# Performance work log

Hardware: AMD Instinct MI355X
Metric: run time of the kernel (lower is better)

## Reference

```python
import jax, jax.numpy as jnp
import numpy as np

N = 50000   # nodes
E = 600000  # directed edges
B = 128     # graphs
IN = 128
H = 128
K = 30      # sort-pool k
C_OUT = 32
KER = 5
OUT_DIM = 10
L_OUT = K - KER + 1  # 26


def setup_inputs() -> dict:
    key = jax.random.key(0)
    ks = jax.random.split(key, 12)
    s = 0.05
    return {
        "x": jax.random.normal(ks[0], (N, IN), jnp.float32),
        "edge_index": jax.random.randint(ks[1], (2, E), 0, N),
        "batch": jnp.sort(jax.random.randint(ks[2], (N,), 0, B)),
        "W0": jax.random.normal(ks[3], (IN, H), jnp.float32) * s,
        "b0": jnp.zeros((H,), jnp.float32),
        "W1": jax.random.normal(ks[4], (H, H), jnp.float32) * s,
        "b1": jnp.zeros((H,), jnp.float32),
        "W2": jax.random.normal(ks[5], (H, H), jnp.float32) * s,
        "b2": jnp.zeros((H,), jnp.float32),
        "conv_w": jax.random.normal(ks[6], (C_OUT, H, KER), jnp.float32) * s,
        "conv_b": jnp.zeros((C_OUT,), jnp.float32),
        "lin1_w": jax.random.normal(ks[7], (C_OUT * L_OUT, H), jnp.float32) * s,
        "lin1_b": jnp.zeros((H,), jnp.float32),
        "lin2_w": jax.random.normal(ks[8], (H, OUT_DIM), jnp.float32) * s,
        "lin2_b": jnp.zeros((OUT_DIM,), jnp.float32),
    }


def reference(x, edge_index, batch, W0, b0, W1, b1, W2, b2,
              conv_w, conv_b, lin1_w, lin1_b, lin2_w, lin2_b):
    # --- GCN normalization (A + I, symmetric deg^-1/2) ---
    loops = jnp.arange(N)
    row = jnp.concatenate([edge_index[0], loops])  # source
    col = jnp.concatenate([edge_index[1], loops])  # target (aggregation side)
    deg = jax.ops.segment_sum(jnp.ones_like(col, dtype=x.dtype), col, num_segments=N)
    dinv = jax.lax.rsqrt(jnp.maximum(deg, 1.0))
    norm = dinv[row] * dinv[col]  # [E+N]

    def gcn(h, W, b):
        hw = h @ W                                            # [N,H]
        msg = hw[row] * norm[:, None]                         # gather [E+N,H]
        return jax.ops.segment_sum(msg, col, num_segments=N) + b

    h = jax.nn.relu(gcn(x, W0, b0))
    h = jax.nn.relu(gcn(h, W1, b1))
    h = jax.nn.relu(gcn(h, W2, b2))

    # --- SortAggregation: per-graph sort by last channel (desc), top-K, zero-pad ---
    last = h[:, -1]
    order = jnp.lexsort((-last, batch))  # primary: batch, secondary: last desc
    hs = h[order]
    bs = batch[order]
    counts = jax.ops.segment_sum(jnp.ones((N,), jnp.int32), batch, num_segments=B)
    starts = jnp.cumsum(counts) - counts  # exclusive prefix sum
    rank = jnp.arange(N) - starts[bs]     # within-graph rank after sort
    r = jnp.where(rank < K, rank, K)      # overflow bucket K is discarded
    pooled = jnp.zeros((B, K + 1, H), h.dtype).at[bs, r].add(hs)[:, :K]  # [B,K,H]

    # --- conv1d head (NCH layout, matches torch view/transpose) ---
    xc = jnp.transpose(pooled, (0, 2, 1))  # [B,H,K]
    y = jax.lax.conv_general_dilated(xc, conv_w, (1,), "VALID",
                                     dimension_numbers=("NCH", "OIH", "NCH"))
    y = jax.nn.relu(y + conv_b[None, :, None])  # [B,C_OUT,L_OUT]
    y = y.reshape(B, -1)
    y = jax.nn.relu(y @ lin1_w + lin1_b)
    return y @ lin2_w + lin2_b  # [B,OUT_DIM]
```

## Files before the change

kernel.cpp:

```cpp
#include <hip/hip_runtime.h>
#include <math.h>

#define Nn 50000
#define Ee 600000
#define Bg 128
#define Hd 128
#define Kt 30
#define CO 32
#define KW 5
#define LOUT 26
#define CAP 2048
#define SCB 196
#define MMB 782

typedef float v2f __attribute__((ext_vector_type(2)));
typedef short bf16x8 __attribute__((ext_vector_type(8)));
typedef float f32x4 __attribute__((ext_vector_type(4)));

__device__ __forceinline__ unsigned short bfr(float v) {
    unsigned u = __builtin_bit_cast(unsigned, v);
    unsigned r = (u + 0x7FFFu + ((u >> 16) & 1u)) >> 16;
    return (unsigned short)r;
}
__device__ __forceinline__ float bff(unsigned short h) {
    unsigned u = ((unsigned)h) << 16;
    return __builtin_bit_cast(float, u);
}

__global__ void countpack_kernel(const int* __restrict__ ei, const int* __restrict__ batch,
                            int* __restrict__ deg_i, int* __restrict__ bstart,
                            const float* __restrict__ conv_w, float* __restrict__ wT2,
                            const float* __restrict__ W0, const float* __restrict__ W1,
                            const float* __restrict__ W2,
                            ushort* __restrict__ Bph, ushort* __restrict__ Bpm,
                            ushort* __restrict__ Bpl) {
    int i = blockIdx.x * 256 + threadIdx.x;
    if (i < Ee) atomicAdd(&deg_i[ei[Ee + i]], 1);
    if (i < Nn) {
        int b = batch[i];
        if (i == 0) bstart[b] = 0;
        else if (batch[i - 1] != b) bstart[b] = i;
    }
    if (i == 0) bstart[Bg] = Nn;
    if (i < CO * KW * Hd) {
        int ci = i & 127;
        int r = i >> 7;
        int o = r / KW, k = r - o * KW;
        wT2[i] = conv_w[((size_t)o * Hd + ci) * KW + k];
    }
    if (i < 3 * 2048) {
        int l = i >> 11;
        int r = i & 2047;
        int kc = r >> 9;
        int n = (r >> 6) & 7;
        int lane = r & 63;
        int m = lane & 15, kq = lane >> 4;
        const float* W = (l == 0) ? W0 : (l == 1) ? W1 : W2;
        int col = n * 16 + m;
        size_t off = ((size_t)l * 2048 + (size_t)((kc * 8 + n) * 64 + lane)) * 8;
#pragma unroll
        for (int j = 0; j < 8; ++j) {
            float v = W[(size_t)(kc * 32 + kq * 8 + j) * Hd + col];
            unsigned short h = bfr(v);
            float r1 = v - bff(h);
            unsigned short mid = bfr(r1);
            Bph[off + j] = h;
            Bpm[off + j] = mid;
            Bpl[off + j] = bfr(r1 - bff(mid));
        }
    }
}

__global__ __launch_bounds__(256) void scanBC2_kernel(const int* __restrict__ deg_i,
                            int* __restrict__ row_ptr, float* __restrict__ dinv,
                            int* __restrict__ bstart) {
    __shared__ int ls[256];
    __shared__ int boffS;
    int tid = threadIdx.x;
    int b = blockIdx.x;
    int s = 0;
    for (int k = 0; k < b; ++k)
        s += deg_i[k * 256 + tid] + 1;
    ls[tid] = s;
    __syncthreads();
    for (int off = 128; off > 0; off >>= 1) {
        if (tid < off) ls[tid] += ls[tid + off];
        __syncthreads();
    }
    if (tid == 0) boffS = ls[0];
    __syncthreads();
    int boff = boffS;
    int i = b * 256 + tid;
    int v2 = 0;
    if (i < Nn) {
        int raw = deg_i[i];
        v2 = raw + 1;
        dinv[i] = 1.0f / sqrtf((float)(raw + 2));
    }
    ls[tid] = v2;
    __syncthreads();
    for (int off = 1; off < 256; off <<= 1) {
        int t = (tid >= off) ? ls[tid - off] : 0;
        __syncthreads();
        ls[tid] += t;
        __syncthreads();
    }
    if (i < Nn) row_ptr[i + 1] = ls[tid] + boff;
    if (i == 0) row_ptr[0] = 0;
    if (b == 0 && tid == 0) {
        for (int bb = Bg - 1; bb >= 0; --bb)
            if (bstart[bb] == -1) bstart[bb] = bstart[bb + 1];
    }
}

__device__ __forceinline__ void mmx_body(int bid, int tid,
                            const float* __restrict__ Hin,
                            const ushort* __restrict__ Bph, const ushort* __restrict__ Bpm,
                            const ushort* __restrict__ Bpl,
                            const float* __restrict__ dinv, float* __restrict__ hw) {
    int w = tid >> 6, lane = tid & 63;
    int m = lane & 15, kq = lane >> 4;
    int rowA = bid * 64 + w * 16 + m;
    bool va = rowA < Nn;
    const float* ap = Hin + (size_t)rowA * Hd;
    f32x4 acc[8];
#pragma unroll
    for (int n = 0; n < 8; ++n) acc[n] = (f32x4)0.f;
#pragma unroll
    for (int kc = 0; kc < 4; ++kc) {
        bf16x8 a0 = (bf16x8)0, a1 = (bf16x8)0, a2 = (bf16x8)0;
        if (va) {
            float av[8];
            *(float4*)&av[0] = *(const float4*)(ap + kc * 32 + kq * 8);
            *(float4*)&av[4] = *(const float4*)(ap + kc * 32 + kq * 8 + 4);
#pragma unroll
            for (int j = 0; j < 8; ++j) {
                unsigned short h = bfr(av[j]);
                float r1 = av[j] - bff(h);
                unsigned short mid = bfr(r1);
                a0[j] = (short)h;
                a1[j] = (short)mid;
                a2[j] = (short)bfr(r1 - bff(mid));
            }
        }
        const ushort* bhp = Bph + (size_t)((kc * 8) * 64 + lane) * 8;
        const ushort* bmp = Bpm + (size_t)((kc * 8) * 64 + lane) * 8;
        const ushort* blp = Bpl + (size_t)((kc * 8) * 64 + lane) * 8;
#pragma unroll
        for (int n = 0; n < 8; ++n) {
            bf16x8 b0 = *(const bf16x8*)(bhp + (size_t)n * 64 * 8);
            bf16x8 b1 = *(const bf16x8*)(bmp + (size_t)n * 64 * 8);
            bf16x8 b2 = *(const bf16x8*)(blp + (size_t)n * 64 * 8);
            acc[n] = __builtin_amdgcn_mfma_f32_16x16x32_bf16(a0, b0, acc[n], 0, 0, 0);
            acc[n] = __builtin_amdgcn_mfma_f32_16x16x32_bf16(a1, b0, acc[n], 0, 0, 0);
            acc[n] = __builtin_amdgcn_mfma_f32_16x16x32_bf16(a0, b1, acc[n], 0, 0, 0);
            acc[n] = __builtin_amdgcn_mfma_f32_16x16x32_bf16(a1, b1, acc[n], 0, 0, 0);
            acc[n] = __builtin_amdgcn_mfma_f32_16x16x32_bf16(a2, b0, acc[n], 0, 0, 0);
            acc[n] = __builtin_amdgcn_mfma_f32_16x16x32_bf16(a0, b2, acc[n], 0, 0, 0);
        }
    }
    int rbase = bid * 64 + w * 16 + kq * 4;
#pragma unroll
    for (int reg = 0; reg < 4; ++reg) {
        int r = rbase + reg;
        if (r < Nn) {
            float s = dinv[r];
#pragma unroll
            for (int n = 0; n < 8; ++n)
                hw[(size_t)r * Hd + n * 16 + m] = acc[n][reg] * s;
        }
    }
}

__global__ __launch_bounds__(256) void mmxfill_kernel(const float* __restrict__ Hin,
                            const ushort* __restrict__ Bph, const ushort* __restrict__ Bpm,
                            const ushort* __restrict__ Bpl,
                            const float* __restrict__ dinv, float* __restrict__ hw,
                            const int* __restrict__ ei, const int* __restrict__ row_ptr,
                            int* __restrict__ cnt, int* __restrict__ csr_src) {
    if (blockIdx.x < MMB) {
        mmx_body(blockIdx.x, threadIdx.x, Hin, Bph, Bpm, Bpl, dinv, hw);
    } else {
        int e = (blockIdx.x - MMB) * 256 + threadIdx.x;
        if (e < Ee) {
            int c = ei[Ee + e];
            int r = ei[e];
            int p = row_ptr[c] + atomicAdd(&cnt[c], 1) + 1;
            csr_src[p] = r;
        }
    }
}

__global__ __launch_bounds__(256) void aggmm_kernel(const float* __restrict__ hwin,
                            const int* __restrict__ row_ptr, const int* __restrict__ csr_src,
                            const float* __restrict__ dinv, const float* __restrict__ bias,
                            const ushort* __restrict__ Bph, const ushort* __restrict__ Bpm,
                            const ushort* __restrict__ Bpl,
                            float* __restrict__ hwout) {
    __shared__ __align__(16) float At[64][132];
    int tid = threadIdx.x;
    int w = tid >> 6, lane = tid & 63;
    int bid = blockIdx.x;
    const v2f* hw2 = (const v2f*)hwin;
    v2f bv = ((const v2f*)bias)[lane];
    for (int t = 0; t < 16; ++t) {
        int rl = w * 16 + t;
        int node = bid * 64 + rl;
        v2f o = (v2f)0.f;
        if (node < Nn) {
            v2f a0 = hw2[(size_t)node * 64 + lane];
            v2f a1 = (v2f)0.f, a2 = (v2f)0.f, a3 = (v2f)0.f;
            int e0 = row_ptr[node], e1 = row_ptr[node + 1];
            int e = e0;
            for (; e + 3 < e1; e += 4) {
                int s0 = __builtin_nontemporal_load(csr_src + e);
                int s1 = __builtin_nontemporal_load(csr_src + e + 1);
                int s2 = __builtin_nontemporal_load(csr_src + e + 2);
                int s3 = __builtin_nontemporal_load(csr_src + e + 3);
                a0 += hw2[(size_t)s0 * 64 + lane];
                a1 += hw2[(size_t)s1 * 64 + lane];
                a2 += hw2[(size_t)s2 * 64 + lane];
                a3 += hw2[(size_t)s3 * 64 + lane];
            }
            for (; e < e1; ++e) {
                int s0 = __builtin_nontemporal_load(csr_src + e);
                a0 += hw2[(size_t)s0 * 64 + lane];
            }
            v2f acc = (a0 + a1) + (a2 + a3);
            float d = dinv[node];
            o.x = fmaxf(fmaf(d, acc.x, bv.x), 0.f);
            o.y = fmaxf(fmaf(d, acc.y, bv.y), 0.f);
        }
        *(v2f*)&At[rl][lane * 2] = o;
    }
    int m = lane & 15, kq = lane >> 4;
    f32x4 acc[8];
#pragma unroll
    for (int n = 0; n < 8; ++n) acc[n] = (f32x4)0.f;
    const float* arow = &At[w * 16 + m][0];
#pragma unroll
    for (int kc = 0; kc < 4; ++kc) {
        bf16x8 a0, a1, a2;
        float av[8];
        *(float4*)&av[0] = *(const float4*)(arow + kc * 32 + kq * 8);
        *(float4*)&av[4] = *(const float4*)(arow + kc * 32 + kq * 8 + 4);
#pragma unroll
        for (int j = 0; j < 8; ++j) {
            unsigned short h = bfr(av[j]);
            float r1 = av[j] - bff(h);
            unsigned short mid = bfr(r1);
            a0[j] = (short)h;
            a1[j] = (short)mid;
            a2[j] = (short)bfr(r1 - bff(mid));
        }
        const ushort* bhp = Bph + (size_t)((kc * 8) * 64 + lane) * 8;
        const ushort* bmp = Bpm + (size_t)((kc * 8) * 64 + lane) * 8;
        const ushort* blp = Bpl + (size_t)((kc * 8) * 64 + lane) * 8;
#pragma unroll
        for (int n = 0; n < 8; ++n) {
            bf16x8 b0 = *(const bf16x8*)(bhp + (size_t)n * 64 * 8);
            bf16x8 b1 = *(const bf16x8*)(bmp + (size_t)n * 64 * 8);
            bf16x8 b2 = *(const bf16x8*)(blp + (size_t)n * 64 * 8);
            acc[n] = __builtin_amdgcn_mfma_f32_16x16x32_bf16(a0, b0, acc[n], 0, 0, 0);
            acc[n] = __builtin_amdgcn_mfma_f32_16x16x32_bf16(a1, b0, acc[n], 0, 0, 0);
            acc[n] = __builtin_amdgcn_mfma_f32_16x16x32_bf16(a0, b1, acc[n], 0, 0, 0);
            acc[n] = __builtin_amdgcn_mfma_f32_16x16x32_bf16(a1, b1, acc[n], 0, 0, 0);
            acc[n] = __builtin_amdgcn_mfma_f32_16x16x32_bf16(a2, b0, acc[n], 0, 0, 0);
            acc[n] = __builtin_amdgcn_mfma_f32_16x16x32_bf16(a0, b2, acc[n], 0, 0, 0);
        }
    }
    int rbase = bid * 64 + w * 16 + kq * 4;
#pragma unroll
    for (int reg = 0; reg < 4; ++reg) {
        int r = rbase + reg;
        if (r < Nn) {
            float s = dinv[r];
#pragma unroll
            for (int n = 0; n < 8; ++n)
                hwout[(size_t)r * Hd + n * 16 + m] = acc[n][reg] * s;
        }
    }
}

__global__ __launch_bounds__(256) void agg_kernel(const float* __restrict__ hw,
                            const int* __restrict__ row_ptr, const int* __restrict__ csr_src,
                            const float* __restrict__ dinv, const float* __restrict__ bias,
                            float* __restrict__ hout) {
    int node = blockIdx.x * 4 + (threadIdx.x >> 6);
    if (node >= Nn) return;
    int lane = threadIdx.x & 63;
    const v2f* hw2 = (const v2f*)hw;
    v2f a0 = hw2[(size_t)node * 64 + lane];
    v2f a1 = 0.f, a2 = 0.f, a3 = 0.f;
    int e0 = row_ptr[node], e1 = row_ptr[node + 1];
    int e = e0;
    for (; e + 3 < e1; e += 4) {
        int s0 = __builtin_nontemporal_load(csr_src + e);
        int s1 = __builtin_nontemporal_load(csr_src + e + 1);
        int s2 = __builtin_nontemporal_load(csr_src + e + 2);
        int s3 = __builtin_nontemporal_load(csr_src + e + 3);
        a0 += hw2[(size_t)s0 * 64 + lane];
        a1 += hw2[(size_t)s1 * 64 + lane];
        a2 += hw2[(size_t)s2 * 64 + lane];
        a3 += hw2[(size_t)s3 * 64 + lane];
    }
    for (; e < e1; ++e) {
        int s0 = __builtin_nontemporal_load(csr_src + e);
        a0 += hw2[(size_t)s0 * 64 + lane];
    }
    v2f acc = (a0 + a1) + (a2 + a3);
    float d = dinv[node];
    v2f bv = ((const v2f*)bias)[lane];
    v2f o;
    o.x = fmaxf(fmaf(d, acc.x, bv.x), 0.f);
    o.y = fmaxf(fmaf(d, acc.y, bv.y), 0.f);
    ((v2f*)hout)[(size_t)node * 64 + lane] = o;
}

__global__ __launch_bounds__(1024) void tail_kernel(const float* __restrict__ h,
                            const int* __restrict__ bstart,
                            const float* __restrict__ wT2, const float* __restrict__ conv_b,
                            const float* __restrict__ l1w, const float* __restrict__ l1b,
                            const float* __restrict__ l2w, const float* __restrict__ l2b,
                            float* __restrict__ out) {
    __shared__ float vals[CAP];
    __shared__ float xcl[Kt][130];
    __shared__ float fl[CO * LOUT];
    __shared__ float pz[8][Hd];
    __shared__ float z[Hd];
    __shared__ int selS[Kt];
    int b = blockIdx.x, tid = threadIdx.x;

    int s0 = bstart[b], s1 = bstart[b + 1];
    int n = s1 - s0;
    int nc = n < CAP ? n : CAP;
    if (tid < Kt) selS[tid] = -1;
    for (int j = tid; j < nc; j += 1024)
        vals[j] = h[(size_t)(s0 + j) * Hd + (Hd - 1)];
    __syncthreads();

    for (int j = tid; j < nc; j += 1024) {
        float vj = vals[j];
        int rank = 0;
        for (int i = 0; i < nc; ++i) {
            float vi = vals[i];
            rank += (vi > vj || (vi == vj && i < j)) ? 1 : 0;
        }
        if (rank < Kt) selS[rank] = s0 + j;
    }
    __syncthreads();

    for (int i = tid; i < Kt * Hd; i += 1024) {
        int t = i >> 7, c = i & 127;
        int s = selS[t];
        xcl[t][c] = (s >= 0) ? h[(size_t)s * Hd + c] : 0.f;
    }
    __syncthreads();
    if (tid < CO * LOUT) {
        int o = tid / LOUT, t = tid - o * LOUT;
        float acc = conv_b[o];
#pragma unroll
        for (int k = 0; k < KW; ++k) {
            const float* xr = &xcl[t + k][0];
            const float* wr = wT2 + ((size_t)o * KW + k) * Hd;
#pragma unroll 8
            for (int c4 = 0; c4 < 32; ++c4) {
                float2 xa = *(const float2*)(xr + c4 * 4);
                float2 xb = *(const float2*)(xr + c4 * 4 + 2);
                float4 wv = *(const float4*)(wr + c4 * 4);
                acc = fmaf(xa.x, wv.x, acc);
                acc = fmaf(xa.y, wv.y, acc);
                acc = fmaf(xb.x, wv.z, acc);
                acc = fmaf(xb.y, wv.w, acc);
            }
        }
        fl[tid] = fmaxf(acc, 0.f);
    }
    __syncthreads();
    int hh = tid & 127, chunk = tid >> 7;
    int m0 = chunk * 104;
    float acc = 0.f;
    const float* lw = l1w + (size_t)m0 * Hd + hh;
#pragma unroll 8
    for (int m = 0; m < 104; ++m)
        acc = fmaf(fl[m0 + m], lw[(size_t)m * Hd], acc);
    pz[chunk][hh] = acc;
    __syncthreads();
    if (tid < Hd) {
        float a = l1b[tid];
#pragma unroll
        for (int q = 0; q < 8; ++q) a += pz[q][tid];
        z[tid] = fmaxf(a, 0.f);
    }
    __syncthreads();
    if (tid < 10) {
        float a2 = l2b[tid];
        for (int j = 0; j < Hd; ++j)
            a2 = fmaf(z[j], l2w[j * 10 + tid], a2);
        out[b * 10 + tid] = a2;
    }
}

extern "C" void kernel_launch(void* const* d_in, const int* in_sizes, int n_in,
                              void* d_out, int out_size, void* d_ws, size_t ws_size,
                              hipStream_t stream) {
    const float* x      = (const float*)d_in[0];
    const int*   ei     = (const int*)d_in[1];
    const int*   batch  = (const int*)d_in[2];
    const float* W0     = (const float*)d_in[3];
    const float* b0     = (const float*)d_in[4];
    const float* W1     = (const float*)d_in[5];
    const float* b1     = (const float*)d_in[6];
    const float* W2     = (const float*)d_in[7];
    const float* b2     = (const float*)d_in[8];
    const float* conv_w = (const float*)d_in[9];
    const float* conv_b = (const float*)d_in[10];
    const float* l1w    = (const float*)d_in[11];
    const float* l1b    = (const float*)d_in[12];
    const float* l2w    = (const float*)d_in[13];
    const float* l2b    = (const float*)d_in[14];
    float* out = (float*)d_out;

    int* wsI = (int*)d_ws;
    size_t off = 0;
    int*   deg_i   = wsI + off; off += Nn;
    int*   cnt     = wsI + off; off += Nn;
    int*   bstart  = wsI + off; off += 132;
    int*   row_ptr = wsI + off; off += 50004;
    float* dinv    = (float*)(wsI + off); off += Nn;
    int*   csr_src = wsI + off; off += Ee;
    off = (off + 3) & ~(size_t)3;
    ushort* Bph  = (ushort*)(wsI + off); off += 3 * 16384 / 2;
    ushort* Bpm  = (ushort*)(wsI + off); off += 3 * 16384 / 2;
    ushort* Bpl  = (ushort*)(wsI + off); off += 3 * 16384 / 2;
    float* hw    = (float*)(wsI + off); off += (size_t)Nn * Hd;
    float* hbuf  = (float*)(wsI + off); off += (size_t)Nn * Hd;
    float* wT2   = (float*)(wsI + off); off += CO * KW * Hd;

    hipMemsetAsync(deg_i, 0xFF, (size_t)(Nn + Nn + 132) * 4, stream);
    countpack_kernel<<<(Ee + 255) / 256, 256, 0, stream>>>(ei, batch, deg_i, bstart,
        conv_w, wT2, W0, W1, W2, Bph, Bpm, Bpl);
    scanBC2_kernel<<<SCB, 256, 0, stream>>>(deg_i, row_ptr, dinv, bstart);
    dim3 aggGrid((Nn + 3) / 4);
    mmxfill_kernel<<<MMB + (Ee + 255) / 256, 256, 0, stream>>>(x, Bph, Bpm, Bpl,
        dinv, hw, ei, row_ptr, cnt, csr_src);
    aggmm_kernel<<<MMB, 256, 0, stream>>>(hw, row_ptr, csr_src, dinv, b0,
        Bph + 16384, Bpm + 16384, Bpl + 16384, hbuf);
    aggmm_kernel<<<MMB, 256, 0, stream>>>(hbuf, row_ptr, csr_src, dinv, b1,
        Bph + 32768, Bpm + 32768, Bpl + 32768, hw);
    agg_kernel<<<aggGrid, 256, 0, stream>>>(hw, row_ptr, csr_src, dinv, b2, hbuf);
    tail_kernel<<<Bg, 1024, 0, stream>>>(hbuf, bstart, wT2, conv_b,
                                         l1w, l1b, l2w, l2b, out);
}
```

Before: 466.7 us.

## Aggregate directly in MFMA A-operand layout, removing LDS staging in aggmm

The fused aggregate+matmul kernel now has each lane accumulate neighbour rows for the node and k-slice it will later feed to the MFMA A operand. This removes the shared-memory tile and its write/read round trip. Each lane now does eight 16-byte loads per neighbour, and each wave handles 16 nodes in parallel instead of looping over 16 nodes serially. The cost is more registers per lane, a less coalesced gather pattern (16 lanes reading different rows), and load imbalance between nodes of different degree within a wave.

```diff
diff --git a/kernel.cpp b/kernel.cpp
--- a/kernel.cpp
+++ b/kernel.cpp
@@ -197,57 +197,60 @@
                             const ushort* __restrict__ Bph, const ushort* __restrict__ Bpm,
                             const ushort* __restrict__ Bpl,
                             float* __restrict__ hwout) {
-    __shared__ __align__(16) float At[64][132];
     int tid = threadIdx.x;
     int w = tid >> 6, lane = tid & 63;
+    int m = lane & 15, kq = lane >> 4;
     int bid = blockIdx.x;
-    const v2f* hw2 = (const v2f*)hwin;
-    v2f bv = ((const v2f*)bias)[lane];
-    for (int t = 0; t < 16; ++t) {
-        int rl = w * 16 + t;
-        int node = bid * 64 + rl;
-        v2f o = (v2f)0.f;
-        if (node < Nn) {
-            v2f a0 = hw2[(size_t)node * 64 + lane];
-            v2f a1 = (v2f)0.f, a2 = (v2f)0.f, a3 = (v2f)0.f;
-            int e0 = row_ptr[node], e1 = row_ptr[node + 1];
-            int e = e0;
-            for (; e + 3 < e1; e += 4) {
-                int s0 = __builtin_nontemporal_load(csr_src + e);
-                int s1 = __builtin_nontemporal_load(csr_src + e + 1);
-                int s2 = __builtin_nontemporal_load(csr_src + e + 2);
-                int s3 = __builtin_nontemporal_load(csr_src + e + 3);
-                a0 += hw2[(size_t)s0 * 64 + lane];
-                a1 += hw2[(size_t)s1 * 64 + lane];
-                a2 += hw2[(size_t)s2 * 64 + lane];
-                a3 += hw2[(size_t)s3 * 64 + lane];
+    int node = bid * 64 + w * 16 + m;
+    bool va = node < Nn;
+    f32x4 s[8];
+#pragma unroll
+    for (int i = 0; i < 8; ++i) s[i] = (f32x4)0.f;
+    if (va) {
+        const float* base = hwin + (size_t)node * Hd + kq * 8;
+#pragma unroll
+        for (int kc = 0; kc < 4; ++kc) {
+            s[kc * 2]     = *(const f32x4*)(base + kc * 32);
+            s[kc * 2 + 1] = *(const f32x4*)(base + kc * 32 + 4);
+        }
+        int e0 = row_ptr[node], e1 = row_ptr[node + 1];
+        int src = (e0 < e1) ? __builtin_nontemporal_load(csr_src + e0) : 0;
+        for (int e = e0; e < e1; ++e) {
+            int nsrc = (e + 1 < e1) ? __builtin_nontemporal_load(csr_src + e + 1) : 0;
+            const float* sp = hwin + (size_t)src * Hd + kq * 8;
+#pragma unroll
+            for (int kc = 0; kc < 4; ++kc) {
+                f32x4 t0 = *(const f32x4*)(sp + kc * 32);
+                f32x4 t1 = *(const f32x4*)(sp + kc * 32 + 4);
+                s[kc * 2]     += t0;
+                s[kc * 2 + 1] += t1;
             }
-            for (; e < e1; ++e) {
-                int s0 = __builtin_nontemporal_load(csr_src + e);
-                a0 += hw2[(size_t)s0 * 64 + lane];
+            src = nsrc;
+        }
+        float d = dinv[node];
+        const float* bp = bias + kq * 8;
+#pragma unroll
+        for (int kc = 0; kc < 4; ++kc) {
+            f32x4 b0 = *(const f32x4*)(bp + kc * 32);
+            f32x4 b1 = *(const f32x4*)(bp + kc * 32 + 4);
+#pragma unroll
+            for (int j = 0; j < 4; ++j) {
+                s[kc * 2][j]     = fmaxf(fmaf(d, s[kc * 2][j],     b0[j]), 0.f);
+                s[kc * 2 + 1][j] = fmaxf(fmaf(d, s[kc * 2 + 1][j], b1[j]), 0.f);
             }
-            v2f acc = (a0 + a1) + (a2 + a3);
-            float d = dinv[node];
-            o.x = fmaxf(fmaf(d, acc.x, bv.x), 0.f);
-            o.y = fmaxf(fmaf(d, acc.y, bv.y), 0.f);
-        }
-        *(v2f*)&At[rl][lane * 2] = o;
-    }
-    int m = lane & 15, kq = lane >> 4;
+        }
+    }
     f32x4 acc[8];
 #pragma unroll
     for (int n = 0; n < 8; ++n) acc[n] = (f32x4)0.f;
-    const float* arow = &At[w * 16 + m][0];
 #pragma unroll
     for (int kc = 0; kc < 4; ++kc) {
         bf16x8 a0, a1, a2;
-        float av[8];
-        *(float4*)&av[0] = *(const float4*)(arow + kc * 32 + kq * 8);
-        *(float4*)&av[4] = *(const float4*)(arow + kc * 32 + kq * 8 + 4);
 #pragma unroll
         for (int j = 0; j < 8; ++j) {
-            unsigned short h = bfr(av[j]);
-            float r1 = av[j] - bff(h);
+            float v = (j < 4) ? s[kc * 2][j] : s[kc * 2 + 1][j - 4];
+            unsigned short h = bfr(v);
+            float r1 = v - bff(h);
             unsigned short mid = bfr(r1);
             a0[j] = (short)h;
             a1[j] = (short)mid;
@@ -274,10 +277,10 @@
     for (int reg = 0; reg < 4; ++reg) {
         int r = rbase + reg;
         if (r < Nn) {
-            float s = dinv[r];
+            float sc = dinv[r];
 #pragma unroll
             for (int n = 0; n < 8; ++n)
-                hwout[(size_t)r * Hd + n * 16 + m] = acc[n][reg] * s;
+                hwout[(size_t)r * Hd + n * 16 + m] = acc[n][reg] * sc;
         }
     }
 }
```

New measurement: 453.6 us. -2.8%, faster.
